# Optimization experiments

Hardware: AMD Instinct MI355X
Metric: run time of the kernel (lower is better)

## Reference

```python
import jax, jax.numpy as jnp
import numpy as np
import math

B, S, E, H, FF = 2, 2048, 1024, 16, 4096
HD = E // H
EPS = 1e-6


def layer_norm(x, gamma, beta):
    mu = jnp.mean(x, axis=-1, keepdims=True)
    var = jnp.mean(jnp.square(x - mu), axis=-1, keepdims=True)
    return (x - mu) * jax.lax.rsqrt(var + EPS) * gamma + beta


def setup_inputs() -> dict:
    key = jax.random.key(0)
    ks = jax.random.split(key, 8)
    x_embeds = jax.random.normal(ks[0], (B, S, E), dtype=jnp.float32)
    # causal mask: True means masked (j > i), broadcastable over batch/heads
    mask = jnp.triu(jnp.ones((S, S), dtype=bool), k=1)[None, None]
    sc = 1.0 / math.sqrt(E)
    w_kqv = jax.random.normal(ks[1], (3 * E, E), dtype=jnp.float32) * sc
    w_o = jax.random.normal(ks[2], (E, E), dtype=jnp.float32) * sc
    w_up = jax.random.normal(ks[3], (FF, E), dtype=jnp.float32) * sc
    b_up = jnp.zeros((FF,), dtype=jnp.float32)
    w_down = jax.random.normal(ks[4], (E, FF), dtype=jnp.float32) / math.sqrt(FF)
    b_down = jnp.zeros((E,), dtype=jnp.float32)
    g1 = jnp.ones((E,), dtype=jnp.float32)
    b1 = jnp.zeros((E,), dtype=jnp.float32)
    g2 = jnp.ones((E,), dtype=jnp.float32)
    b2 = jnp.zeros((E,), dtype=jnp.float32)
    return {"x_embeds": x_embeds, "mask": mask, "w_kqv": w_kqv, "w_o": w_o,
            "w_up": w_up, "b_up": b_up, "w_down": w_down, "b_down": b_down,
            "g1": g1, "b1": b1, "g2": g2, "b2": b2}


def reference(x_embeds, mask, w_kqv, w_o, w_up, b_up, w_down, b_down, g1, b1, g2, b2):
    b, s = x_embeds.shape[0], x_embeds.shape[1]
    # --- attention ---
    kqv = x_embeds @ w_kqv.T                      # [B,S,3E]
    kqv = kqv.reshape(b, s, 3, H, HD).transpose(0, 3, 2, 1, 4)  # [B,H,3,S,HD]
    xk, xq, xv = kqv[:, :, 0], kqv[:, :, 1], kqv[:, :, 2]
    attn = jnp.einsum('bhqd,bhkd->bhqk', xq, xk) / math.sqrt(HD)
    attn = jnp.where(mask, -jnp.inf, attn)
    attn = jax.nn.softmax(attn, axis=-1)
    out = jnp.einsum('bhqk,bhkd->bhqd', attn, xv)  # [B,H,S,HD]
    out = out.transpose(0, 2, 1, 3).reshape(b, s, E)
    out = out @ w_o.T
    x = layer_norm(out + x_embeds, g1, b1)
    # --- ffnn ---
    h = jax.nn.relu(x @ w_up.T + b_up)
    h = h @ w_down.T + b_down
    return layer_norm(h + x, g2, b2)
```

## Files before the change

### kernel.cpp

```cpp
#include <hip/hip_runtime.h>
#include <stdint.h>

#define B_ 2
#define S_ 2048
#define E_ 1024
#define H_ 16
#define HD_ 64
#define FF_ 4096
#define M_ 4096
#define LOG2E_ 1.44269504f

typedef short bf16x8 __attribute__((ext_vector_type(8)));
typedef float f32x4  __attribute__((ext_vector_type(4)));
typedef short shortx4 __attribute__((ext_vector_type(4)));

#define MFMA16(a,b,c) __builtin_amdgcn_mfma_f32_16x16x32_bf16(a,b,c,0,0,0)

__device__ __forceinline__ short f2bf(float f) {
  uint32_t u = __builtin_bit_cast(uint32_t, f);
  u += 0x7fffu + ((u >> 16) & 1u);
  return (short)(u >> 16);
}
__device__ __forceinline__ float bf2f(short b) {
  uint32_t u = ((uint32_t)(uint16_t)b) << 16;
  return __builtin_bit_cast(float, u);
}
__device__ __forceinline__ float exp2_hw(float x) {
  float r;
  asm("v_exp_f32 %0, %1" : "=v"(r) : "v"(x));
  return r;
}

template<int CTRL>
__device__ __forceinline__ float dpp_ror(float x) {
  return __builtin_bit_cast(float,
    __builtin_amdgcn_update_dpp(0, __builtin_bit_cast(int, x), CTRL, 0xF, 0xF, true));
}
__device__ __forceinline__ float dpp_max16(float v) {
  v = fmaxf(v, dpp_ror<0x128>(v));
  v = fmaxf(v, dpp_ror<0x124>(v));
  v = fmaxf(v, dpp_ror<0x122>(v));
  v = fmaxf(v, dpp_ror<0x121>(v));
  return v;
}
__device__ __forceinline__ float dpp_sum16(float v) {
  v += dpp_ror<0x128>(v);
  v += dpp_ror<0x124>(v);
  v += dpp_ror<0x122>(v);
  v += dpp_ror<0x121>(v);
  return v;
}

#define GLDS16(g, l) __builtin_amdgcn_global_load_lds( \
    (const __attribute__((address_space(1))) unsigned int*)(g), \
    (__attribute__((address_space(3))) unsigned int*)(l), 16, 0, 0)

__global__ void cast_all(const float* __restrict__ x, const float* __restrict__ wkqv,
                         const float* __restrict__ wo, const float* __restrict__ wup,
                         const float* __restrict__ wdown,
                         short* __restrict__ xb, short* __restrict__ wkqvb,
                         short* __restrict__ wob, short* __restrict__ wupb,
                         short* __restrict__ wdownb) {
  const int stride = gridDim.x * blockDim.x;
  for (int i = blockIdx.x * blockDim.x + threadIdx.x; i < 4194304; i += stride) {
    const int e = i << 2;
    const float* src; short* dst; int off;
    if (e < 4194304)       { src = x;     dst = xb;     off = e; }
    else if (e < 7340032)  { src = wkqv;  dst = wkqvb;  off = e - 4194304; }
    else if (e < 8388608)  { src = wo;    dst = wob;    off = e - 7340032; }
    else if (e < 12582912) { src = wup;   dst = wupb;   off = e - 8388608; }
    else                   { src = wdown; dst = wdownb; off = e - 12582912; }
    float4 v = *(const float4*)(src + off);
    shortx4 o;
    o.x = f2bf(v.x); o.y = f2bf(v.y); o.z = f2bf(v.z); o.w = f2bf(v.w);
    *(shortx4*)(dst + off) = o;
  }
}

template<int SK, int EPI, typename OutT>
__global__ __launch_bounds__(256) void gemm_bt(
    const short* __restrict__ A, const short* __restrict__ Bw,
    OutT* __restrict__ C0, OutT* __restrict__ C1, const float* __restrict__ bias,
    int M, int N, int K)
{
  __shared__ short Al[128 * 32];
  __shared__ short Bl[128 * 32];
  const int tid  = threadIdx.x;
  const int w    = tid >> 6, lane = tid & 63;
  const int ntiles = N >> 7;
  const int nwg = gridDim.x;
  const int bid = blockIdx.x;
  const int swz = (bid & 7) * (nwg >> 3) + (bid >> 3);
  const int tn = swz % ntiles, tm = swz / ntiles;
  const int m0 = tm << 7, n0 = tn << 7;
  const int wr = (w >> 1) << 6, wc = (w & 1) << 6;
  const int lr = lane & 15, lk = (lane >> 4) << 3;
  const int ra = lane >> 2, colA = (lane & 3) << 3;

  const int kper = K / SK;
  const int kbeg = (SK > 1) ? (int)blockIdx.y * kper : 0;
  const int kend = kbeg + kper;
  OutT* __restrict__ C = (SK > 1 && blockIdx.y) ? C1 : C0;

  f32x4 acc[4][4] = {};

  for (int k0 = kbeg; k0 < kend; k0 += 32) {
    __syncthreads();
    #pragma unroll
    for (int i = 0; i < 2; ++i) {
      const int ch = w + (i << 2);
      GLDS16(A  + (size_t)(m0 + ch * 16 + ra) * K + k0 + colA, &Al[ch * 512]);
      GLDS16(Bw + (size_t)(n0 + ch * 16 + ra) * K + k0 + colA, &Bl[ch * 512]);
    }
    __syncthreads();
    bf16x8 af[4], bfr[4];
    #pragma unroll
    for (int i = 0; i < 4; ++i)
      af[i] = *(const bf16x8*)&Al[(wr + i * 16 + lr) * 32 + lk];
    #pragma unroll
    for (int j = 0; j < 4; ++j)
      bfr[j] = *(const bf16x8*)&Bl[(wc + j * 16 + lr) * 32 + lk];
    #pragma unroll
    for (int i = 0; i < 4; ++i)
      #pragma unroll
      for (int j = 0; j < 4; ++j)
        acc[i][j] = MFMA16(af[i], bfr[j], acc[i][j]);
  }

  const int lg = lane >> 4;
  #pragma unroll
  for (int j = 0; j < 4; ++j) {
    const int col = n0 + wc + j * 16 + lr;
    float bv = 0.f;
    if constexpr (SK == 1 && EPI != 0) bv = bias[col];
    #pragma unroll
    for (int i = 0; i < 4; ++i) {
      #pragma unroll
      for (int r = 0; r < 4; ++r) {
        const int row = m0 + wr + i * 16 + lg * 4 + r;
        float v = acc[i][j][r] + bv;
        if constexpr (SK == 1 && EPI == 1) v = fmaxf(v, 0.f);
        if constexpr (sizeof(OutT) == 2) C[(size_t)row * N + col] = f2bf(v);
        else                             C[(size_t)row * N + col] = v;
      }
    }
  }
}

__global__ __launch_bounds__(256) void attn_kernel(
    const short* __restrict__ kqv, short* __restrict__ out)
{
  __shared__ short Kt[64][72];
  __shared__ short Vt[64][72];
  __shared__ short Pl[4][16][72];

  const int tid = threadIdx.x, w = tid >> 6, lane = tid & 63;
  const int p = blockIdx.x;
  const int bh = blockIdx.y;
  const int b = bh >> 4, h = bh & 15;
  const int q0lo = p << 6, q0hi = (31 - p) << 6;
  const int nkb = 32 - p;
  const int lr = lane & 15, lg = lane >> 4;

  const size_t rowlo = (size_t)(b * S_ + q0lo + w * 16 + lr) * 3072 + 1024 + h * 64;
  const size_t rowhi = (size_t)(b * S_ + q0hi + w * 16 + lr) * 3072 + 1024 + h * 64;
  bf16x8 qlo[2], qhi[2];
  qlo[0] = *(const bf16x8*)&kqv[rowlo + lg * 8];
  qlo[1] = *(const bf16x8*)&kqv[rowlo + 32 + lg * 8];
  qhi[0] = *(const bf16x8*)&kqv[rowhi + lg * 8];
  qhi[1] = *(const bf16x8*)&kqv[rowhi + 32 + lg * 8];
  #pragma unroll
  for (int ks = 0; ks < 2; ++ks)
    #pragma unroll
    for (int e = 0; e < 8; ++e) {
      qlo[ks][e] = f2bf(bf2f(qlo[ks][e]) * 0.125f);
      qhi[ks][e] = f2bf(bf2f(qhi[ks][e]) * 0.125f);
    }

  f32x4 aclo[4] = {}, achi[4] = {};
  float mlo[4], llo[4], mhi[4], lhi[4];
  #pragma unroll
  for (int r = 0; r < 4; ++r) { mlo[r] = mhi[r] = -1e30f; llo[r] = lhi[r] = 0.f; }

  const int skk = tid >> 3;
  const int sc  = (tid & 7) << 3;
  const int vws = (tid & 7) << 3;

  for (int kbi = 0; kbi < nkb; ++kbi) {
    const int kb = kbi << 6;
    #pragma unroll
    for (int i = 0; i < 2; ++i) {
      const int krow = skk + i * 32;
      const size_t gb = (size_t)(b * S_ + kb + krow) * 3072 + h * 64 + sc;
      *(bf16x8*)&Kt[krow][sc] = *(const bf16x8*)&kqv[gb];
      bf16x8 vv = *(const bf16x8*)&kqv[gb + 2048];
      const int kc = krow ^ vws;
      #pragma unroll
      for (int e = 0; e < 8; ++e) Vt[sc + e][kc] = vv[e];
    }
    __syncthreads();

    auto process = [&](const bf16x8 (&qf)[2], f32x4 (&acc)[4],
                       float (&m_run)[4], float (&l_run)[4], int q0) {
      f32x4 sacc[4] = {};
      __builtin_amdgcn_s_setprio(1);
      #pragma unroll
      for (int jt = 0; jt < 4; ++jt) {
        #pragma unroll
        for (int ks = 0; ks < 2; ++ks) {
          bf16x8 kf = *(const bf16x8*)&Kt[jt * 16 + lr][ks * 32 + lg * 8];
          sacc[jt] = MFMA16(qf[ks], kf, sacc[jt]);
        }
      }
      __builtin_amdgcn_s_setprio(0);
      const bool full = (kb + 63 <= q0 + w * 16);
      float rmax[4];
      if (full) {
        #pragma unroll
        for (int r = 0; r < 4; ++r)
          rmax[r] = fmaxf(fmaxf(sacc[0][r], sacc[1][r]), fmaxf(sacc[2][r], sacc[3][r]));
      } else {
        #pragma unroll
        for (int r = 0; r < 4; ++r) rmax[r] = -1e30f;
        #pragma unroll
        for (int jt = 0; jt < 4; ++jt) {
          const int kpos = kb + jt * 16 + lr;
          #pragma unroll
          for (int r = 0; r < 4; ++r) {
            const int qrow = q0 + w * 16 + lg * 4 + r;
            float v = (kpos <= qrow) ? sacc[jt][r] : -1e30f;
            sacc[jt][r] = v;
            rmax[r] = fmaxf(rmax[r], v);
          }
        }
      }
      #pragma unroll
      for (int r = 0; r < 4; ++r) rmax[r] = dpp_max16(rmax[r]);
      int need = 0;
      #pragma unroll
      for (int r = 0; r < 4; ++r) need |= (rmax[r] > m_run[r] + 8.f) ? 1 : 0;
      if (__any(need)) {
        #pragma unroll
        for (int r = 0; r < 4; ++r) {
          const float mn = fmaxf(m_run[r], rmax[r]);
          const float al = exp2_hw((m_run[r] - mn) * LOG2E_);
          m_run[r] = mn;
          l_run[r] *= al;
          #pragma unroll
          for (int dt = 0; dt < 4; ++dt) acc[dt][r] *= al;
        }
      }
      float m2[4], rsum[4];
      #pragma unroll
      for (int r = 0; r < 4; ++r) { m2[r] = m_run[r] * LOG2E_; rsum[r] = 0.f; }
      #pragma unroll
      for (int jt = 0; jt < 4; ++jt)
        #pragma unroll
        for (int r = 0; r < 4; ++r) {
          const float pv = exp2_hw(__builtin_fmaf(sacc[jt][r], LOG2E_, -m2[r]));
          sacc[jt][r] = pv;
          rsum[r] += pv;
        }
      #pragma unroll
      for (int r = 0; r < 4; ++r) { rsum[r] = dpp_sum16(rsum[r]); l_run[r] += rsum[r]; }
      #pragma unroll
      for (int jt = 0; jt < 4; ++jt) {
        uint32_t w01, w23;
        asm("v_cvt_pk_bf16_f32 %0, %1, %2" : "=v"(w01) : "v"(sacc[jt][0]), "v"(sacc[jt][1]));
        asm("v_cvt_pk_bf16_f32 %0, %1, %2" : "=v"(w23) : "v"(sacc[jt][2]), "v"(sacc[jt][3]));
        Pl[w][lg * 4 + 0][jt * 16 + lr] = (short)(w01 & 0xffffu);
        Pl[w][lg * 4 + 1][jt * 16 + lr] = (short)(w01 >> 16);
        Pl[w][lg * 4 + 2][jt * 16 + lr] = (short)(w23 & 0xffffu);
        Pl[w][lg * 4 + 3][jt * 16 + lr] = (short)(w23 >> 16);
      }
      bf16x8 pa[2];
      pa[0] = *(const bf16x8*)&Pl[w][lr][lg * 8];
      pa[1] = *(const bf16x8*)&Pl[w][lr][32 + lg * 8];
      __builtin_amdgcn_s_setprio(1);
      #pragma unroll
      for (int dt = 0; dt < 4; ++dt) {
        const int vswz = (2 * dt + (lr >> 3)) << 3;
        #pragma unroll
        for (int ks = 0; ks < 2; ++ks) {
          bf16x8 vb = *(const bf16x8*)&Vt[dt * 16 + lr][(ks * 32 + lg * 8) ^ vswz];
          acc[dt] = MFMA16(pa[ks], vb, acc[dt]);
        }
      }
      __builtin_amdgcn_s_setprio(0);
    };

    process(qhi, achi, mhi, lhi, q0hi);
    if (kb <= q0lo + w * 16 + 15) process(qlo, aclo, mlo, llo, q0lo);
    __syncthreads();
  }

  #pragma unroll
  for (int dt = 0; dt < 4; ++dt) {
    #pragma unroll
    for (int r = 0; r < 4; ++r) {
      const int d = h * 64 + dt * 16 + lr;
      const int qlo_row = q0lo + w * 16 + lg * 4 + r;
      const int qhi_row = q0hi + w * 16 + lg * 4 + r;
      out[(size_t)(b * S_ + qlo_row) * E_ + d] = f2bf(aclo[dt][r] / llo[r]);
      out[(size_t)(b * S_ + qhi_row) * E_ + d] = f2bf(achi[dt][r] / lhi[r]);
    }
  }
}

template<int FINAL>
__global__ __launch_bounds__(256) void ln_kernel(
    const float* __restrict__ y0, const float* __restrict__ y1,
    const float* __restrict__ bias, const void* __restrict__ res,
    const float* __restrict__ gam, const float* __restrict__ bet,
    void* __restrict__ outp)
{
  const int row = blockIdx.x, tid = threadIdx.x, lane = tid & 63, w = tid >> 6;
  float4 a = ((const float4*)(y0 + (size_t)row * E_))[tid];
  float4 c = ((const float4*)(y1 + (size_t)row * E_))[tid];
  float r[4] = {a.x + c.x, a.y + c.y, a.z + c.z, a.w + c.w};
  if constexpr (FINAL) {
    float4 bi = ((const float4*)bias)[tid];
    shortx4 rb = ((const shortx4*)((const short*)res + (size_t)row * E_))[tid];
    r[0] += bi.x + bf2f(rb.x); r[1] += bi.y + bf2f(rb.y);
    r[2] += bi.z + bf2f(rb.z); r[3] += bi.w + bf2f(rb.w);
  } else {
    float4 rv = ((const float4*)((const float*)res + (size_t)row * E_))[tid];
    r[0] += rv.x; r[1] += rv.y; r[2] += rv.z; r[3] += rv.w;
  }
  float s  = r[0] + r[1] + r[2] + r[3];
  float ss = r[0]*r[0] + r[1]*r[1] + r[2]*r[2] + r[3]*r[3];
  #pragma unroll
  for (int m = 32; m >= 1; m >>= 1) { s += __shfl_xor(s, m); ss += __shfl_xor(ss, m); }
  __shared__ float red[8];
  if (lane == 0) { red[w] = s; red[4 + w] = ss; }
  __syncthreads();
  s  = red[0] + red[1] + red[2] + red[3];
  ss = red[4] + red[5] + red[6] + red[7];
  const float mu  = s * (1.f / E_);
  const float var = ss * (1.f / E_) - mu * mu;
  const float rs  = rsqrtf(var + 1e-6f);
  float4 gv = ((const float4*)gam)[tid];
  float4 bv = ((const float4*)bet)[tid];
  float o0 = (r[0] - mu) * rs * gv.x + bv.x;
  float o1 = (r[1] - mu) * rs * gv.y + bv.y;
  float o2 = (r[2] - mu) * rs * gv.z + bv.z;
  float o3 = (r[3] - mu) * rs * gv.w + bv.w;
  if constexpr (FINAL) {
    float4 o; o.x = o0; o.y = o1; o.z = o2; o.w = o3;
    ((float4*)((float*)outp + (size_t)row * E_))[tid] = o;
  } else {
    shortx4 o; o.x = f2bf(o0); o.y = f2bf(o1); o.z = f2bf(o2); o.w = f2bf(o3);
    ((shortx4*)((short*)outp + (size_t)row * E_))[tid] = o;
  }
}

extern "C" void kernel_launch(void* const* d_in, const int* in_sizes, int n_in,
                              void* d_out, int out_size, void* d_ws, size_t ws_size,
                              hipStream_t stream) {
  const float* x      = (const float*)d_in[0];
  const float* w_kqv  = (const float*)d_in[2];
  const float* w_o    = (const float*)d_in[3];
  const float* w_up   = (const float*)d_in[4];
  const float* b_up   = (const float*)d_in[5];
  const float* w_down = (const float*)d_in[6];
  const float* b_down = (const float*)d_in[7];
  const float* g1     = (const float*)d_in[8];
  const float* b1     = (const float*)d_in[9];
  const float* g2     = (const float*)d_in[10];
  const float* b2     = (const float*)d_in[11];
  float* out = (float*)d_out;

  char* ws = (char*)d_ws;
  short* xb     = (short*)(ws);
  short* wkqvb  = (short*)(ws + ((size_t)8  << 20));
  short* wob    = (short*)(ws + ((size_t)14 << 20));
  short* wupb   = (short*)(ws + ((size_t)16 << 20));
  short* wdownb = (short*)(ws + ((size_t)24 << 20));
  short* kqv    = (short*)(ws + ((size_t)32 << 20));
  float* proj0  = (float*)(ws + ((size_t)32 << 20));
  float* proj1  = (float*)(ws + ((size_t)48 << 20));
  short* hbuf   = (short*)(ws + ((size_t)32 << 20));
  short* attno  = (short*)(ws + ((size_t)64 << 20));
  short* xln    = (short*)(ws + ((size_t)72 << 20));
  float* down0  = (float*)(ws);
  float* down1  = (float*)(ws + ((size_t)80 << 20));

  cast_all<<<2048, 256, 0, stream>>>(x, w_kqv, w_o, w_up, w_down,
                                     xb, wkqvb, wob, wupb, wdownb);

  gemm_bt<1, 0, short><<<24 * 32, 256, 0, stream>>>(xb, wkqvb, kqv, nullptr, nullptr, M_, 3 * E_, E_);
  attn_kernel<<<dim3(16, B_ * H_), 256, 0, stream>>>(kqv, attno);
  gemm_bt<2, 0, float><<<dim3(256, 2), 256, 0, stream>>>(attno, wob, proj0, proj1, nullptr, M_, E_, E_);
  ln_kernel<0><<<M_, 256, 0, stream>>>(proj0, proj1, nullptr, x, g1, b1, xln);
  gemm_bt<1, 1, short><<<32 * 32, 256, 0, stream>>>(xln, wupb, hbuf, nullptr, b_up, M_, FF_, E_);
  gemm_bt<2, 0, float><<<dim3(256, 2), 256, 0, stream>>>(hbuf, wdownb, down0, down1, nullptr, M_, E_, FF_);
  ln_kernel<1><<<M_, 256, 0, stream>>>(down0, down1, b_down, xln, g2, b2, out);
}
```

Measured before the change: 277.2 us.

## Double-buffer LDS tiles in bf16 GEMM to overlap global loads with MFMA

The GEMM kernel now uses two LDS buffers for the A and B tiles. It issues the global-to-LDS loads for the next K-step before computing the current one and waits with an explicit vmcnt instead of a full __syncthreads. This is meant to hide global memory latency behind the MFMA work. In exchange it doubles LDS use per block, which may lower occupancy, and relies on hand-placed waitcnt and barrier ordering that must be correct.

```diff
diff --git a/kernel.cpp b/kernel.cpp
--- a/kernel.cpp
+++ b/kernel.cpp
@@ -83,8 +83,8 @@
     OutT* __restrict__ C0, OutT* __restrict__ C1, const float* __restrict__ bias,
     int M, int N, int K)
 {
-  __shared__ short Al[128 * 32];
-  __shared__ short Bl[128 * 32];
+  __shared__ short Al[2][128 * 32];
+  __shared__ short Bl[2][128 * 32];
   const int tid  = threadIdx.x;
   const int w    = tid >> 6, lane = tid & 63;
   const int ntiles = N >> 7;
@@ -99,32 +99,53 @@
 
   const int kper = K / SK;
   const int kbeg = (SK > 1) ? (int)blockIdx.y * kper : 0;
-  const int kend = kbeg + kper;
+  const int T = kper >> 5;
   OutT* __restrict__ C = (SK > 1 && blockIdx.y) ? C1 : C0;
 
+  const short* Ag0 = A  + (size_t)(m0 + w * 16 + ra) * K + colA;
+  const short* Ag1 = A  + (size_t)(m0 + (w + 4) * 16 + ra) * K + colA;
+  const short* Bg0 = Bw + (size_t)(n0 + w * 16 + ra) * K + colA;
+  const short* Bg1 = Bw + (size_t)(n0 + (w + 4) * 16 + ra) * K + colA;
+
   f32x4 acc[4][4] = {};
 
-  for (int k0 = kbeg; k0 < kend; k0 += 32) {
-    __syncthreads();
-    #pragma unroll
-    for (int i = 0; i < 2; ++i) {
-      const int ch = w + (i << 2);
-      GLDS16(A  + (size_t)(m0 + ch * 16 + ra) * K + k0 + colA, &Al[ch * 512]);
-      GLDS16(Bw + (size_t)(n0 + ch * 16 + ra) * K + k0 + colA, &Bl[ch * 512]);
+  {
+    const int k0 = kbeg;
+    GLDS16(Ag0 + k0, &Al[0][w * 512]);
+    GLDS16(Ag1 + k0, &Al[0][(w + 4) * 512]);
+    GLDS16(Bg0 + k0, &Bl[0][w * 512]);
+    GLDS16(Bg1 + k0, &Bl[0][(w + 4) * 512]);
+  }
+
+  for (int it = 0; it < T; ++it) {
+    const int buf = it & 1;
+    if (it + 1 < T) {
+      const int k1 = kbeg + ((it + 1) << 5);
+      GLDS16(Ag0 + k1, &Al[buf ^ 1][w * 512]);
+      GLDS16(Ag1 + k1, &Al[buf ^ 1][(w + 4) * 512]);
+      GLDS16(Bg0 + k1, &Bl[buf ^ 1][w * 512]);
+      GLDS16(Bg1 + k1, &Bl[buf ^ 1][(w + 4) * 512]);
+      asm volatile("s_waitcnt vmcnt(4)" ::: "memory");
+    } else {
+      asm volatile("s_waitcnt vmcnt(0)" ::: "memory");
     }
-    __syncthreads();
+    __builtin_amdgcn_sched_barrier(0);
+    __builtin_amdgcn_s_barrier();
+
     bf16x8 af[4], bfr[4];
     #pragma unroll
     for (int i = 0; i < 4; ++i)
-      af[i] = *(const bf16x8*)&Al[(wr + i * 16 + lr) * 32 + lk];
+      af[i] = *(const bf16x8*)&Al[buf][(wr + i * 16 + lr) * 32 + lk];
     #pragma unroll
     for (int j = 0; j < 4; ++j)
-      bfr[j] = *(const bf16x8*)&Bl[(wc + j * 16 + lr) * 32 + lk];
+      bfr[j] = *(const bf16x8*)&Bl[buf][(wc + j * 16 + lr) * 32 + lk];
     #pragma unroll
     for (int i = 0; i < 4; ++i)
       #pragma unroll
       for (int j = 0; j < 4; ++j)
         acc[i][j] = MFMA16(af[i], bfr[j], acc[i][j]);
+
+    __builtin_amdgcn_s_barrier();
   }
 
   const int lg = lane >> 4;
```

Measured after the change: 257.4 us. 1.08x faster.
